# Performance work log

Measured on AMD Instinct MI355X. Metric: run time of the kernel, lower is better.

Reference implementation:

```python
import jax, jax.numpy as jnp
import numpy as np

B, S, L, H, VIN, VOUT = 64, 64, 64, 256, 10000, 10000


def setup_inputs() -> dict:
    key = jax.random.key(0)
    ks = jax.random.split(key, 14)
    f = lambda k, shp: jax.random.normal(k, shp, dtype=jnp.float32) * 0.05
    return {
        "X": f(ks[0], (B, S, VIN)),
        "ground_truth": jax.random.randint(ks[1], (B, L), 0, VOUT, dtype=jnp.int32),
        "enc_Wih": f(ks[2], (3 * H, VIN)),
        "enc_Whh": f(ks[3], (3 * H, H)),
        "enc_bih": f(ks[4], (3 * H,)),
        "enc_bhh": f(ks[5], (3 * H,)),
        "att_w": f(ks[6], (2 * H,)),
        "att_b": f(ks[7], ()),
        "dec_Wih": f(ks[8], (3 * H, H + VOUT)),
        "dec_Whh": f(ks[9], (3 * H, H)),
        "dec_bih": f(ks[10], (3 * H,)),
        "dec_bhh": f(ks[11], (3 * H,)),
        "out_W": f(ks[12], (VOUT, H)),
        "out_b": f(ks[13], (VOUT,)),
    }


def gru_cell(h, x, Wih, Whh, bih, bhh):
    # PyTorch GRU cell: gates ordered (r, z, n)
    gi = x @ Wih.T + bih          # [B, 3H]
    gh = h @ Whh.T + bhh          # [B, 3H]
    ir, iz, inn = jnp.split(gi, 3, axis=-1)
    hr, hz, hn = jnp.split(gh, 3, axis=-1)
    r = jax.nn.sigmoid(ir + hr)
    z = jax.nn.sigmoid(iz + hz)
    n = jnp.tanh(inn + r * hn)
    return (1.0 - z) * n + z * h


def reference(X, ground_truth, enc_Wih, enc_Whh, enc_bih, enc_bhh,
              att_w, att_b, dec_Wih, dec_Whh, dec_bih, dec_bhh, out_W, out_b):
    b = X.shape[0]
    h_dim = enc_Whh.shape[1]
    vout = out_W.shape[0]

    # ---- encoder GRU over time (time-major scan) ----
    Xs = jnp.transpose(X, (1, 0, 2))                      # [S, B, VIN]
    h0 = jnp.zeros((b, h_dim), X.dtype)

    def enc_step(h, x):
        h2 = gru_cell(h, x, enc_Wih, enc_Whh, enc_bih, enc_bhh)
        return h2, h2

    h_last, enc_h = jax.lax.scan(enc_step, h0, Xs)        # enc_h: [S, B, H]

    # additive attention: logits = relu(W_a [h_dec; enc_h] + b_a)
    w_dec, w_enc = jnp.split(att_w, 2)                    # each [H]
    enc_score = jnp.einsum('sbh,h->sb', enc_h, w_enc)     # precomputed, [S, B]

    gtT = ground_truth.T                                  # [L, B]
    prev0 = jnp.zeros((b, vout), X.dtype)                 # initial one-hot input (zeros)

    def dec_step(carry, gt_i):
        h, prev = carry
        logits = jax.nn.relu(enc_score + h @ w_dec + att_b)   # [S, B]
        wts = jax.nn.softmax(logits, axis=0)                  # softmax over enc positions
        ctx = jnp.einsum('sb,sbh->bh', wts, enc_h)            # [B, H]
        dec_in = jnp.concatenate([ctx, prev], axis=-1)        # [B, H + VOUT]
        h2 = gru_cell(h, dec_in, dec_Wih, dec_Whh, dec_bih, dec_bhh)
        logp = jax.nn.log_softmax(h2 @ out_W.T + out_b, axis=-1)  # [B, VOUT]
        onehot = jax.nn.one_hot(gt_i, vout, dtype=X.dtype)        # teacher forcing
        return (h2, onehot), logp

    _, outs = jax.lax.scan(dec_step, (h_last, prev0), gtT)    # [L, B, VOUT]
    return jnp.transpose(outs, (1, 0, 2))                     # [B, L, VOUT]
```

## Files before the change

kernel.cpp:

```cpp
#include <hip/hip_runtime.h>
#include <hip/hip_bf16.h>
#include <math.h>

#define NB 64
#define NS 64
#define NL 64
#define NH 256
#define G3 768
#define NVIN 10000
#define NVOUT 10000
#define KP2 10240
#define NOUTP 10112

typedef __attribute__((ext_vector_type(8))) short bf16x8;
typedef __attribute__((ext_vector_type(4))) float f32x4;
typedef __attribute__((ext_vector_type(4))) unsigned int u32x4;

__device__ __forceinline__ void gld_lds16(const __hip_bfloat16* g, __hip_bfloat16* l) {
  __builtin_amdgcn_global_load_lds(
      (const __attribute__((address_space(1))) unsigned int*)(const void*)g,
      (__attribute__((address_space(3))) unsigned int*)(void*)l, 16, 0, 0);
}

__device__ __forceinline__ unsigned int f2bf(float f) {
  unsigned int u = __float_as_uint(f);
  return (u + 0x7fff + ((u >> 16) & 1)) >> 16;
}

__device__ __forceinline__ float fast_tanh(float x) {
  float e = __expf(-2.f * x);
  return (1.f - e) / (1.f + e);
}

__global__ __launch_bounds__(256) void k_cvt_pad(
    const float* __restrict__ in, __hip_bfloat16* __restrict__ out,
    int in_rows, int in_cols, int out_cols, int swz) {
  int r = blockIdx.x;
  const float* src = in + (size_t)r * in_cols;
  __hip_bfloat16* dst = out + (size_t)r * out_cols;
  bool live = r < in_rows;
  int sx = swz ? ((r & 7) << 3) : 0;
  for (int c = threadIdx.x * 4; c < out_cols; c += 1024) {
    int cc = (c & ~63) | ((c & 63) ^ sx);
    __hip_bfloat16 v[4];
    if (live && cc + 3 < in_cols) {
      float4 f = *(const float4*)(src + cc);
      v[0] = __float2bfloat16(f.x); v[1] = __float2bfloat16(f.y);
      v[2] = __float2bfloat16(f.z); v[3] = __float2bfloat16(f.w);
    } else {
      v[0] = v[1] = v[2] = v[3] = __float2bfloat16(0.f);
    }
    *(ushort4*)(dst + c) = *(const ushort4*)v;
  }
}

__global__ __launch_bounds__(256) void k_wpack(
    const float* __restrict__ srcA, int strideA,
    const float* __restrict__ srcB, int strideB,
    __hip_bfloat16* __restrict__ out, int total) {
  int idx = blockIdx.x * 256 + threadIdx.x;
  if (idx >= total) return;
  int k = idx & 255, c = (idx >> 8) & 255, f = idx >> 16;
  float v = (f < 3) ? srcA[(size_t)(f * 256 + c) * strideA + k]
                    : srcB[(size_t)((f - 3) * 256 + c) * strideB + k];
  out[idx] = __float2bfloat16(v);
}

__global__ __launch_bounds__(256) void k_gemm_encS(
    const __hip_bfloat16* __restrict__ A, const __hip_bfloat16* __restrict__ B,
    float* __restrict__ P) {
  __shared__ __hip_bfloat16 As[128][64];
  __shared__ __hip_bfloat16 Bs[128][64];
  int t = threadIdx.x;
  int wid = t >> 6, lane = t & 63;
  int m0 = blockIdx.y * 128, n0 = blockIdx.x * 128;
  int wr = wid >> 1, wc = wid & 1;
  int r16 = lane & 15, hi16 = lane >> 4;
  int xr = (r16 & 7) << 4;
  f32x4 acc[4][4] = {};
  int kbeg = blockIdx.z * 2560;
  for (int ks = 0; ks < 40; ++ks) {
    int k0 = kbeg + ks * 64;
    __syncthreads();
#pragma unroll
    for (int is = 0; is < 4; ++is) {
      int off = is * 4096 + t * 16;
      int r = off >> 7, e = (off & 127) >> 1;
      gld_lds16(A + (size_t)(m0 + r) * KP2 + k0 + e, &As[r][e]);
      gld_lds16(B + (size_t)(n0 + r) * KP2 + k0 + e, &Bs[r][e]);
    }
    __syncthreads();
    const char* ab = (const char*)As;
    const char* bb = (const char*)Bs;
#pragma unroll
    for (int kk = 0; kk < 2; ++kk) {
      int ko = kk * 64 + hi16 * 16;
      bf16x8 af[4], bfr[4];
#pragma unroll
      for (int i = 0; i < 4; ++i) {
        af[i]  = *(const bf16x8*)(ab + (wr * 64 + i * 16 + r16) * 128 + (ko ^ xr));
        bfr[i] = *(const bf16x8*)(bb + (wc * 64 + i * 16 + r16) * 128 + (ko ^ xr));
      }
#pragma unroll
      for (int i = 0; i < 4; ++i)
#pragma unroll
        for (int j = 0; j < 4; ++j)
          acc[i][j] = __builtin_amdgcn_mfma_f32_16x16x32_bf16(af[i], bfr[j], acc[i][j], 0, 0, 0);
    }
  }
  float* Pz = P + (size_t)blockIdx.z * 4096 * G3;
#pragma unroll
  for (int i = 0; i < 4; ++i)
#pragma unroll
    for (int j = 0; j < 4; ++j) {
      int ccol = n0 + wc * 64 + j * 16 + r16;
#pragma unroll
      for (int q = 0; q < 4; ++q) {
        int crow = m0 + wr * 64 + i * 16 + hi16 * 4 + q;
        Pz[(size_t)crow * G3 + ccol] = acc[i][j][q];
      }
    }
}

__global__ __launch_bounds__(256) void k_reduce4(
    const float4* __restrict__ P, const float* __restrict__ bias,
    float4* __restrict__ G) {
  int idx = blockIdx.x * 256 + threadIdx.x;
  float4 a = P[idx], b = P[idx + 786432], c = P[idx + 2 * 786432],
         d = P[idx + 3 * 786432];
  float4 bs = *(const float4*)(bias + (idx % 192) * 4);
  float4 o;
  o.x = a.x + b.x + c.x + d.x + bs.x;
  o.y = a.y + b.y + c.y + d.y + bs.y;
  o.z = a.z + b.z + c.z + d.z + bs.z;
  o.w = a.w + b.w + c.w + d.w + bs.w;
  G[idx] = o;
}

__global__ __launch_bounds__(256) void k_gemm_outS(
    const __hip_bfloat16* __restrict__ A, const __hip_bfloat16* __restrict__ B,
    const float* __restrict__ bias, float* __restrict__ C) {
  __shared__ __hip_bfloat16 As[128][64];
  __shared__ __hip_bfloat16 Bs[128][64];
  int t = threadIdx.x;
  int wid = t >> 6, lane = t & 63;
  int m0 = blockIdx.y * 128, n0 = blockIdx.x * 128;
  int wr = wid >> 1, wc = wid & 1;
  int r16 = lane & 15, hi16 = lane >> 4;
  int xr = (r16 & 7) << 4;
  f32x4 acc[4][4] = {};
  for (int k0 = 0; k0 < NH; k0 += 64) {
    __syncthreads();
#pragma unroll
    for (int is = 0; is < 4; ++is) {
      int off = is * 4096 + t * 16;
      int r = off >> 7, e = (off & 127) >> 1;
      gld_lds16(A + (size_t)(m0 + r) * NH + k0 + e, &As[r][e]);
      gld_lds16(B + (size_t)(n0 + r) * NH + k0 + e, &Bs[r][e]);
    }
    __syncthreads();
    const char* ab = (const char*)As;
    const char* bb = (const char*)Bs;
#pragma unroll
    for (int kk = 0; kk < 2; ++kk) {
      int ko = kk * 64 + hi16 * 16;
      bf16x8 af[4], bfr[4];
#pragma unroll
      for (int i = 0; i < 4; ++i) {
        af[i]  = *(const bf16x8*)(ab + (wr * 64 + i * 16 + r16) * 128 + (ko ^ xr));
        bfr[i] = *(const bf16x8*)(bb + (wc * 64 + i * 16 + r16) * 128 + (ko ^ xr));
      }
#pragma unroll
      for (int i = 0; i < 4; ++i)
#pragma unroll
        for (int j = 0; j < 4; ++j)
          acc[i][j] = __builtin_amdgcn_mfma_f32_16x16x32_bf16(af[i], bfr[j], acc[i][j], 0, 0, 0);
    }
  }
#pragma unroll
  for (int i = 0; i < 4; ++i)
#pragma unroll
    for (int j = 0; j < 4; ++j) {
      int ccol = n0 + wc * 64 + j * 16 + r16;
      if (ccol < NVOUT) {
        float bs = bias[ccol];
#pragma unroll
        for (int q = 0; q < 4; ++q) {
          int crow = m0 + wr * 64 + i * 16 + hi16 * 4 + q;
          int l = crow >> 6, b = crow & 63;
          C[((size_t)b * NL + l) * NVOUT + ccol] = acc[i][j][q] + bs;
        }
      }
    }
}

__global__ __launch_bounds__(256) void k_gemm_encw(
    const __hip_bfloat16* __restrict__ A, const __hip_bfloat16* __restrict__ B,
    __hip_bfloat16* __restrict__ CT) {
  __shared__ __hip_bfloat16 As[128][32];
  __shared__ __hip_bfloat16 Bs[128][32];
  int t = threadIdx.x;
  int wid = t >> 6, lane = t & 63;
  int m0 = blockIdx.y * 128, n0 = blockIdx.x * 128;
  int wr = wid >> 1, wc = wid & 1;
  f32x4 acc[4][4] = {};
  for (int k0 = 0; k0 < NH; k0 += 32) {
    __syncthreads();
#pragma unroll
    for (int is = 0; is < 2; ++is) {
      int off = is * 4096 + wid * 1024 + lane * 16;
      int r = off >> 6, cb = (off & 63) >> 1;
      gld_lds16(A + (size_t)(m0 + r) * NH + k0 + cb, &As[r][cb]);
      gld_lds16(B + (size_t)(n0 + r) * NH + k0 + cb, &Bs[r][cb]);
    }
    __syncthreads();
    int r16 = lane & 15, kb = (lane >> 4) * 8;
    bf16x8 af[4], bfr[4];
#pragma unroll
    for (int i = 0; i < 4; ++i) {
      af[i]  = *(const bf16x8*)&As[wr * 64 + i * 16 + r16][kb];
      bfr[i] = *(const bf16x8*)&Bs[wc * 64 + i * 16 + r16][kb];
    }
#pragma unroll
    for (int i = 0; i < 4; ++i)
#pragma unroll
      for (int j = 0; j < 4; ++j)
        acc[i][j] = __builtin_amdgcn_mfma_f32_16x16x32_bf16(af[i], bfr[j], acc[i][j], 0, 0, 0);
  }
  int r16 = lane & 15, rg = lane >> 4;
#pragma unroll
  for (int i = 0; i < 4; ++i)
#pragma unroll
    for (int j = 0; j < 4; ++j) {
      int ccol = n0 + wc * 64 + j * 16 + r16;
#pragma unroll
      for (int q = 0; q < 4; ++q) {
        int crow = m0 + wr * 64 + i * 16 + rg * 4 + q;
        int bb = crow >> 6, ss = crow & 63;
        CT[((size_t)bb * G3 + ccol) * 64 + (ss ^ ((ccol & 7) << 3))] =
            __float2bfloat16(acc[i][j][q]);
      }
    }
}

__global__ __launch_bounds__(256) void k_pregather(
    const float* __restrict__ Wih, const float* __restrict__ bih,
    const int* __restrict__ gt, float* __restrict__ Gdec) {
  int ib = blockIdx.x;
  int i = ib >> 6, b = ib & 63;
  int tok = (i > 0) ? gt[b * NL + (i - 1)] : -1;
  for (int g = threadIdx.x; g < G3; g += 256) {
    float v = bih[g];
    if (tok >= 0) v += Wih[(size_t)g * (NH + NVOUT) + NH + tok];
    Gdec[(size_t)ib * G3 + g] = v;
  }
}

__global__ __launch_bounds__(512) void k_encoder4(
    const float* __restrict__ Gi, const __hip_bfloat16* __restrict__ Wcat,
    const float* __restrict__ bhh, const float* __restrict__ att_w,
    __hip_bfloat16* __restrict__ enchB, float* __restrict__ escoreT) {
  __shared__ float h32[2][256];
  __shared__ __hip_bfloat16 hbf[2][256];
  int t = threadIdx.x, w = t >> 6, lane = t & 63;
  int b = blockIdx.x;
  int r16 = lane & 15, hi16 = lane >> 4;
  bf16x8 wv[3][2][8];
#pragma unroll
  for (int f = 0; f < 3; ++f)
#pragma unroll
    for (int fc = 0; fc < 2; ++fc)
#pragma unroll
      for (int kf = 0; kf < 8; ++kf)
        wv[f][fc][kf] = *(const bf16x8*)(Wcat +
            (((size_t)f * 256 + w * 32 + fc * 16 + r16) * 256 + kf * 32 + hi16 * 8));
  float aw[4];
#pragma unroll
  for (int q = 0; q < 4; ++q) aw[q] = att_w[256 + lane + q * 64];
  if (t < 256) {
    h32[0][t] = 0.f; h32[1][t] = 0.f;
    hbf[0][t] = __float2bfloat16(0.f); hbf[1][t] = __float2bfloat16(0.f);
  }
  __syncthreads();
  int cur = 0;
  for (int s = 0; s < NS; ++s) {
    float gd[3][2];
    if (hi16 == 0) {
#pragma unroll
      for (int f = 0; f < 3; ++f)
#pragma unroll
        for (int fc = 0; fc < 2; ++fc)
          gd[f][fc] = Gi[((size_t)b * 64 + s) * G3 + f * 256 + w * 32 + fc * 16 + lane];
    }
    const char* hb = (const char*)&hbf[cur][0];
    f32x4 acc[3][2] = {};
#pragma unroll
    for (int half = 0; half < 2; ++half) {
      bf16x8 ah[4];
#pragma unroll
      for (int kf = 0; kf < 4; ++kf)
        ah[kf] = *(const bf16x8*)(hb + (half * 4 + kf) * 64 + hi16 * 16);
#pragma unroll
      for (int f = 0; f < 3; ++f)
#pragma unroll
        for (int fc = 0; fc < 2; ++fc)
#pragma unroll
          for (int kf = 0; kf < 4; ++kf)
            acc[f][fc] = __builtin_amdgcn_mfma_f32_16x16x32_bf16(
                ah[kf], wv[f][fc][half * 4 + kf], acc[f][fc], 0, 0, 0);
    }
    if (hi16 == 0) {
      int nxt = cur ^ 1;
#pragma unroll
      for (int fc = 0; fc < 2; ++fc) {
        int c = w * 32 + fc * 16 + lane;
        float rr = 1.f / (1.f + __expf(-(gd[0][fc] + acc[0][fc][0] + bhh[c])));
        float zz = 1.f / (1.f + __expf(-(gd[1][fc] + acc[1][fc][0] + bhh[256 + c])));
        float nn = fast_tanh(gd[2][fc] + rr * (acc[2][fc][0] + bhh[512 + c]));
        float hn = (1.f - zz) * nn + zz * h32[cur][c];
        h32[nxt][c] = hn;
        hbf[nxt][c] = __float2bfloat16(hn);
        enchB[((size_t)b * 64 + s) * 256 + c] = __float2bfloat16(hn);
      }
    }
    __syncthreads();
    cur ^= 1;
    if (w == 0) {
      float p = h32[cur][lane] * aw[0] + h32[cur][lane + 64] * aw[1]
              + h32[cur][lane + 128] * aw[2] + h32[cur][lane + 192] * aw[3];
#pragma unroll
      for (int off = 32; off; off >>= 1) p += __shfl_xor(p, off, 64);
      if (lane == 0) escoreT[(size_t)b * 64 + s] = p;
    }
  }
}

__global__ __launch_bounds__(512) void k_decoder6(
    const float* __restrict__ Gdec, const __hip_bfloat16* __restrict__ Wcat6,
    const float* __restrict__ bhh, const __hip_bfloat16* __restrict__ enchB,
    const __hip_bfloat16* __restrict__ ENCWT, const float* __restrict__ escoreT,
    const float* __restrict__ att_w, const float* __restrict__ att_b,
    __hip_bfloat16* __restrict__ dechb) {
  __shared__ __hip_bfloat16 encwT[G3][64];
  __shared__ __hip_bfloat16 hbf[2][256];
  __shared__ float h32[2][256];
  int t = threadIdx.x, w = t >> 6, lane = t & 63;
  int b = blockIdx.x;
  int r16 = lane & 15, hi16 = lane >> 4;
  int cw = w * 32;
  {
    const char* srcb = (const char*)(ENCWT + (size_t)b * G3 * 64);
    char* dstb = (char*)&encwT[0][0];
#pragma unroll
    for (int is = 0; is < 12; ++is) {
      int off = is * 8192 + t * 16;
      gld_lds16((const __hip_bfloat16*)(srcb + off), (__hip_bfloat16*)(dstb + off));
    }
  }
  bf16x8 wv[3][2][8];
#pragma unroll
  for (int f = 0; f < 3; ++f)
#pragma unroll
    for (int fc = 0; fc < 2; ++fc)
#pragma unroll
      for (int kf = 0; kf < 8; ++kf)
        wv[f][fc][kf] = *(const bf16x8*)(Wcat6 +
            (((size_t)(3 + f) * 256 + cw + fc * 16 + r16) * 256 + kf * 32 + hi16 * 8));
  float aw[4];
#pragma unroll
  for (int q = 0; q < 4; ++q) aw[q] = att_w[lane + q * 64];
  float attb = att_b[0];
  float esc = escoreT[(size_t)b * 64 + lane];
  float bh0[2], bh1[2], bh2[2];
#pragma unroll
  for (int fc = 0; fc < 2; ++fc) {
    bh0[fc] = bhh[cw + fc * 16 + r16];
    bh1[fc] = bhh[256 + cw + fc * 16 + r16];
    bh2[fc] = bhh[512 + cw + fc * 16 + r16];
  }
  u32x4 onesu = {0x3F803F80u, 0x3F803F80u, 0x3F803F80u, 0x3F803F80u};
  bf16x8 onesf = __builtin_bit_cast(bf16x8, onesu);
  if (t < 256) {
    float v = __bfloat162float(enchB[((size_t)b * 64 + 63) * 256 + t]);
    h32[0][t] = v;  hbf[0][t] = __float2bfloat16(v);
    h32[1][t] = 0.f; hbf[1][t] = __float2bfloat16(0.f);
  }
  __syncthreads();
  float hp[2];
  hp[0] = h32[0][cw + r16];
  hp[1] = h32[0][cw + 16 + r16];
  int bs3 = (b & 7) << 3;
  int cur = 0;
  for (int i = 0; i < NL; ++i) {
    float gd0[2], gd1[2], gd2[2];
    if (hi16 == 0) {
      const float* gp = Gdec + ((size_t)i * 64 + b) * G3;
#pragma unroll
      for (int fc = 0; fc < 2; ++fc) {
        gd0[fc] = gp[cw + fc * 16 + r16];
        gd1[fc] = gp[256 + cw + fc * 16 + r16];
        gd2[fc] = gp[512 + cw + fc * 16 + r16];
      }
    }
    const char* hb = (const char*)&hbf[cur][0];
    f32x4 acch[3][2] = {};
#pragma unroll
    for (int half = 0; half < 2; ++half) {
      bf16x8 ah[4];
#pragma unroll
      for (int kf = 0; kf < 4; ++kf)
        ah[kf] = *(const bf16x8*)(hb + (half * 4 + kf) * 64 + hi16 * 16);
#pragma unroll
      for (int f = 0; f < 3; ++f)
#pragma unroll
        for (int fc = 0; fc < 2; ++fc)
#pragma unroll
          for (int kf = 0; kf < 4; ++kf)
            acch[f][fc] = __builtin_amdgcn_mfma_f32_16x16x32_bf16(
                ah[kf], wv[f][fc][half * 4 + kf], acch[f][fc], 0, 0, 0);
    }
    float p = h32[cur][lane] * aw[0] + h32[cur][lane + 64] * aw[1]
            + h32[cur][lane + 128] * aw[2] + h32[cur][lane + 192] * aw[3];
#pragma unroll
    for (int off = 32; off; off >>= 1) p += __shfl_xor(p, off, 64);
    float lg = fmaxf(esc + p + attb, 0.f);
    float e = __expf(lg);
    bf16x8 af_[2];
#pragma unroll
    for (int kf = 0; kf < 2; ++kf) {
      u32x4 tmp;
#pragma unroll
      for (int j = 0; j < 4; ++j) {
        int src = hi16 * 8 + kf * 32 + 2 * j;
        tmp[j] = f2bf(__shfl(e, src, 64)) | (f2bf(__shfl(e, src + 1, 64)) << 16);
      }
      af_[kf] = __builtin_bit_cast(bf16x8, tmp);
    }
    f32x4 smacc = {};
    smacc = __builtin_amdgcn_mfma_f32_16x16x32_bf16(af_[0], onesf, smacc, 0, 0, 0);
    smacc = __builtin_amdgcn_mfma_f32_16x16x32_bf16(af_[1], onesf, smacc, 0, 0, 0);
    f32x4 acci[3][2] = {};
    const char* eb = (const char*)&encwT[0][0];
#pragma unroll
    for (int g = 0; g < 3; ++g)
#pragma unroll
      for (int fc = 0; fc < 2; ++fc) {
        int cloc = g * 256 + cw + fc * 16 + r16;
        int xb = (cloc & 7) << 4;
#pragma unroll
        for (int kf = 0; kf < 2; ++kf) {
          bf16x8 bfrag = *(const bf16x8*)(eb + cloc * 128 + ((kf * 64 + hi16 * 16) ^ xb));
          acci[g][fc] = __builtin_amdgcn_mfma_f32_16x16x32_bf16(
              af_[kf], bfrag, acci[g][fc], 0, 0, 0);
        }
      }
    if (hi16 == 0) {
      float rn = 1.f / smacc[0];
      int nxt = cur ^ 1;
#pragma unroll
      for (int fc = 0; fc < 2; ++fc) {
        int c = cw + fc * 16 + r16;
        float rr = 1.f / (1.f + __expf(-(gd0[fc] + acci[0][fc][0] * rn + acch[0][fc][0] + bh0[fc])));
        float zz = 1.f / (1.f + __expf(-(gd1[fc] + acci[1][fc][0] * rn + acch[1][fc][0] + bh1[fc])));
        float nn = fast_tanh(gd2[fc] + acci[2][fc][0] * rn + rr * (acch[2][fc][0] + bh2[fc]));
        float hn = (1.f - zz) * nn + zz * hp[fc];
        hp[fc] = hn;
        h32[nxt][c] = hn;
        hbf[nxt][c] = __float2bfloat16(hn);
        int cs = (c & ~63) | ((c & 63) ^ bs3);
        dechb[((size_t)i * 64 + b) * 256 + cs] = __float2bfloat16(hn);
      }
    }
    __syncthreads();
    cur ^= 1;
  }
}

__global__ __launch_bounds__(256) void k_logsoftmax(float* __restrict__ out) {
  float* x = out + (size_t)blockIdx.x * NVOUT;
  __shared__ float red[256];
  int t = threadIdx.x;
  float4 v[10];
  float mx = -1e30f;
#pragma unroll
  for (int ii = 0; ii < 10; ++ii) {
    int slot = ii * 256 + t;
    if (slot < 2500) {
      v[ii] = *(const float4*)(x + slot * 4);
      mx = fmaxf(mx, fmaxf(fmaxf(v[ii].x, v[ii].y), fmaxf(v[ii].z, v[ii].w)));
    }
  }
  red[t] = mx; __syncthreads();
  for (int off = 128; off; off >>= 1) {
    if (t < off) red[t] = fmaxf(red[t], red[t + off]);
    __syncthreads();
  }
  mx = red[0]; __syncthreads();
  float sm = 0.f;
#pragma unroll
  for (int ii = 0; ii < 10; ++ii) {
    int slot = ii * 256 + t;
    if (slot < 2500)
      sm += __expf(v[ii].x - mx) + __expf(v[ii].y - mx)
          + __expf(v[ii].z - mx) + __expf(v[ii].w - mx);
  }
  red[t] = sm; __syncthreads();
  for (int off = 128; off; off >>= 1) {
    if (t < off) red[t] += red[t + off];
    __syncthreads();
  }
  float lse = mx + logf(red[0]);
#pragma unroll
  for (int ii = 0; ii < 10; ++ii) {
    int slot = ii * 256 + t;
    if (slot < 2500) {
      float4 o; o.x = v[ii].x - lse; o.y = v[ii].y - lse;
      o.z = v[ii].z - lse; o.w = v[ii].w - lse;
      *(float4*)(x + slot * 4) = o;
    }
  }
}

extern "C" void kernel_launch(void* const* d_in, const int* in_sizes, int n_in,
                              void* d_out, int out_size, void* d_ws, size_t ws_size,
                              hipStream_t stream) {
  const float* X        = (const float*)d_in[0];
  const int*   gt       = (const int*)  d_in[1];
  const float* enc_Wih  = (const float*)d_in[2];
  const float* enc_Whh  = (const float*)d_in[3];
  const float* enc_bih  = (const float*)d_in[4];
  const float* enc_bhh  = (const float*)d_in[5];
  const float* att_w    = (const float*)d_in[6];
  const float* att_b    = (const float*)d_in[7];
  const float* dec_Wih  = (const float*)d_in[8];
  const float* dec_Whh  = (const float*)d_in[9];
  const float* dec_bih  = (const float*)d_in[10];
  const float* dec_bhh  = (const float*)d_in[11];
  const float* out_W    = (const float*)d_in[12];
  const float* out_b    = (const float*)d_in[13];
  float* out = (float*)d_out;

  float* p = (float*)d_ws;
  float* Gienc  = p; p += NS * NB * G3;
  float* Gdec   = p; p += NL * NB * G3;
  float* escoreT = p; p += NB * NS;
  __hip_bfloat16* q = (__hip_bfloat16*)p;
  __hip_bfloat16* enchBb = q; q += (size_t)NB * NS * NH;
  __hip_bfloat16* Wcat_e = q; q += (size_t)3 * 256 * 256;
  __hip_bfloat16* Wcat_d = q; q += (size_t)6 * 256 * 256;
  __hip_bfloat16* Xb     = q; q += (size_t)4096 * KP2;
  __hip_bfloat16* Wencb  = q; q += (size_t)G3 * KP2;
  __hip_bfloat16* Woutb  = q; q += (size_t)NOUTP * NH;
  __hip_bfloat16* dechb  = q; q += (size_t)NL * NB * NH;
  __hip_bfloat16* ENCWT  = (__hip_bfloat16*)Gienc;
  float* Pout = (float*)d_out;

  k_cvt_pad<<<4096, 256, 0, stream>>>(X, Xb, 4096, NVIN, KP2, 1);
  k_cvt_pad<<<G3, 256, 0, stream>>>(enc_Wih, Wencb, G3, NVIN, KP2, 1);
  k_cvt_pad<<<NOUTP, 256, 0, stream>>>(out_W, Woutb, NVOUT, NH, NH, 1);
  k_wpack<<<768, 256, 0, stream>>>(enc_Whh, NH, enc_Whh, NH, Wcat_e, 3 * 65536);
  k_wpack<<<1536, 256, 0, stream>>>(dec_Wih, NH + NVOUT, dec_Whh, NH, Wcat_d, 6 * 65536);
  k_pregather<<<NL * NB, 256, 0, stream>>>(dec_Wih, dec_bih, gt, Gdec);

  k_gemm_encS<<<dim3(6, 32, 4), 256, 0, stream>>>(Xb, Wencb, Pout);
  k_reduce4<<<3072, 256, 0, stream>>>((const float4*)Pout, enc_bih, (float4*)Gienc);
  k_encoder4<<<64, 512, 0, stream>>>(Gienc, Wcat_e, enc_bhh, att_w, enchBb, escoreT);
  k_gemm_encw<<<dim3(6, 32), 256, 0, stream>>>(enchBb, Wcat_d, ENCWT);
  k_decoder6<<<64, 512, 0, stream>>>(Gdec, Wcat_d, dec_bhh, enchBb, ENCWT,
                                     escoreT, att_w, att_b, dechb);
  k_gemm_outS<<<dim3(79, 32), 256, 0, stream>>>(dechb, Woutb, out_b, out);
  k_logsoftmax<<<NB * NL, 256, 0, stream>>>(out);
}
```

Measured before the change: 789.4 us.

## Trim serial recurrence critical path in encoder and decoder GRU loops

```diff
diff --git a/kernel.cpp b/kernel.cpp
--- a/kernel.cpp
+++ b/kernel.cpp
@@ -30,6 +30,10 @@
 __device__ __forceinline__ float fast_tanh(float x) {
   float e = __expf(-2.f * x);
   return (1.f - e) / (1.f + e);
+}
+
+__device__ __forceinline__ void lds_barrier() {
+  asm volatile("s_waitcnt lgkmcnt(0)\n\ts_barrier" ::: "memory");
 }
 
 __global__ __launch_bounds__(256) void k_cvt_pad(
@@ -256,15 +260,14 @@
   }
 }
 
-__global__ __launch_bounds__(512) void k_encoder4(
+__global__ __launch_bounds__(512) void k_encoder5(
     const float* __restrict__ Gi, const __hip_bfloat16* __restrict__ Wcat,
-    const float* __restrict__ bhh, const float* __restrict__ att_w,
-    __hip_bfloat16* __restrict__ enchB, float* __restrict__ escoreT) {
-  __shared__ float h32[2][256];
+    const float* __restrict__ bhh, __hip_bfloat16* __restrict__ enchB) {
   __shared__ __hip_bfloat16 hbf[2][256];
   int t = threadIdx.x, w = t >> 6, lane = t & 63;
   int b = blockIdx.x;
   int r16 = lane & 15, hi16 = lane >> 4;
+  int cw = w * 32;
   bf16x8 wv[3][2][8];
 #pragma unroll
   for (int f = 0; f < 3; ++f)
@@ -273,24 +276,31 @@
 #pragma unroll
       for (int kf = 0; kf < 8; ++kf)
         wv[f][fc][kf] = *(const bf16x8*)(Wcat +
-            (((size_t)f * 256 + w * 32 + fc * 16 + r16) * 256 + kf * 32 + hi16 * 8));
-  float aw[4];
-#pragma unroll
-  for (int q = 0; q < 4; ++q) aw[q] = att_w[256 + lane + q * 64];
+            (((size_t)f * 256 + cw + fc * 16 + r16) * 256 + kf * 32 + hi16 * 8));
+  float bh0[2], bh1[2], bh2[2];
+#pragma unroll
+  for (int fc = 0; fc < 2; ++fc) {
+    bh0[fc] = bhh[cw + fc * 16 + r16];
+    bh1[fc] = bhh[256 + cw + fc * 16 + r16];
+    bh2[fc] = bhh[512 + cw + fc * 16 + r16];
+  }
   if (t < 256) {
-    h32[0][t] = 0.f; h32[1][t] = 0.f;
-    hbf[0][t] = __float2bfloat16(0.f); hbf[1][t] = __float2bfloat16(0.f);
+    hbf[0][t] = __float2bfloat16(0.f);
+    hbf[1][t] = __float2bfloat16(0.f);
   }
   __syncthreads();
+  float hp[2] = {0.f, 0.f};
   int cur = 0;
   for (int s = 0; s < NS; ++s) {
-    float gd[3][2];
+    float gd0[2], gd1[2], gd2[2];
     if (hi16 == 0) {
-#pragma unroll
-      for (int f = 0; f < 3; ++f)
-#pragma unroll
-        for (int fc = 0; fc < 2; ++fc)
-          gd[f][fc] = Gi[((size_t)b * 64 + s) * G3 + f * 256 + w * 32 + fc * 16 + lane];
+      const float* gp = Gi + ((size_t)b * 64 + s) * G3;
+#pragma unroll
+      for (int fc = 0; fc < 2; ++fc) {
+        gd0[fc] = gp[cw + fc * 16 + r16];
+        gd1[fc] = gp[256 + cw + fc * 16 + r16];
+        gd2[fc] = gp[512 + cw + fc * 16 + r16];
+      }
     }
     const char* hb = (const char*)&hbf[cur][0];
     f32x4 acc[3][2] = {};
@@ -313,37 +323,46 @@
       int nxt = cur ^ 1;
 #pragma unroll
       for (int fc = 0; fc < 2; ++fc) {
-        int c = w * 32 + fc * 16 + lane;
-        float rr = 1.f / (1.f + __expf(-(gd[0][fc] + acc[0][fc][0] + bhh[c])));
-        float zz = 1.f / (1.f + __expf(-(gd[1][fc] + acc[1][fc][0] + bhh[256 + c])));
-        float nn = fast_tanh(gd[2][fc] + rr * (acc[2][fc][0] + bhh[512 + c]));
-        float hn = (1.f - zz) * nn + zz * h32[cur][c];
-        h32[nxt][c] = hn;
+        int c = cw + fc * 16 + r16;
+        float rr = 1.f / (1.f + __expf(-(gd0[fc] + acc[0][fc][0] + bh0[fc])));
+        float zz = 1.f / (1.f + __expf(-(gd1[fc] + acc[1][fc][0] + bh1[fc])));
+        float nn = fast_tanh(gd2[fc] + rr * (acc[2][fc][0] + bh2[fc]));
+        float hn = (1.f - zz) * nn + zz * hp[fc];
+        hp[fc] = hn;
         hbf[nxt][c] = __float2bfloat16(hn);
         enchB[((size_t)b * 64 + s) * 256 + c] = __float2bfloat16(hn);
       }
     }
-    __syncthreads();
+    lds_barrier();
     cur ^= 1;
-    if (w == 0) {
-      float p = h32[cur][lane] * aw[0] + h32[cur][lane + 64] * aw[1]
-              + h32[cur][lane + 128] * aw[2] + h32[cur][lane + 192] * aw[3];
-#pragma unroll
-      for (int off = 32; off; off >>= 1) p += __shfl_xor(p, off, 64);
-      if (lane == 0) escoreT[(size_t)b * 64 + s] = p;
-    }
-  }
-}
-
-__global__ __launch_bounds__(512) void k_decoder6(
+  }
+}
+
+__global__ __launch_bounds__(256) void k_escoreB(
+    const __hip_bfloat16* __restrict__ enchB, const float* __restrict__ att_w,
+    float* __restrict__ escoreT) {
+  int row = blockIdx.x * 4 + (threadIdx.x >> 6);
+  int lane = threadIdx.x & 63;
+  ushort4 u = *(const ushort4*)(enchB + (size_t)row * 256 + lane * 4);
+  const float* we = att_w + 256 + lane * 4;
+  float p = __uint_as_float((unsigned)u.x << 16) * we[0]
+          + __uint_as_float((unsigned)u.y << 16) * we[1]
+          + __uint_as_float((unsigned)u.z << 16) * we[2]
+          + __uint_as_float((unsigned)u.w << 16) * we[3];
+#pragma unroll
+  for (int off = 32; off; off >>= 1) p += __shfl_xor(p, off, 64);
+  if (lane == 0) escoreT[row] = p;
+}
+
+__global__ __launch_bounds__(512) void k_decoder7(
     const float* __restrict__ Gdec, const __hip_bfloat16* __restrict__ Wcat6,
     const float* __restrict__ bhh, const __hip_bfloat16* __restrict__ enchB,
     const __hip_bfloat16* __restrict__ ENCWT, const float* __restrict__ escoreT,
     const float* __restrict__ att_w, const float* __restrict__ att_b,
     __hip_bfloat16* __restrict__ dechb) {
-  __shared__ __hip_bfloat16 encwT[G3][64];
+  __shared__ __hip_bfloat16 encwT[G3 + 8][64];
   __shared__ __hip_bfloat16 hbf[2][256];
-  __shared__ float h32[2][256];
+  __shared__ float psumL[2][8];
   int t = threadIdx.x, w = t >> 6, lane = t & 63;
   int b = blockIdx.x;
   int r16 = lane & 15, hi16 = lane >> 4;
@@ -357,6 +376,10 @@
       gld_lds16((const __hip_bfloat16*)(srcb + off), (__hip_bfloat16*)(dstb + off));
     }
   }
+  {
+    unsigned* op = (unsigned*)&encwT[768][0];
+    if (t < 32) op[t] = 0x3F803F80u;
+  }
   bf16x8 wv[3][2][8];
 #pragma unroll
   for (int f = 0; f < 3; ++f)
@@ -366,9 +389,7 @@
       for (int kf = 0; kf < 8; ++kf)
         wv[f][fc][kf] = *(const bf16x8*)(Wcat6 +
             (((size_t)(3 + f) * 256 + cw + fc * 16 + r16) * 256 + kf * 32 + hi16 * 8));
-  float aw[4];
-#pragma unroll
-  for (int q = 0; q < 4; ++q) aw[q] = att_w[lane + q * 64];
+  float wd0 = att_w[cw + r16], wd1 = att_w[cw + 16 + r16];
   float attb = att_b[0];
   float esc = escoreT[(size_t)b * 64 + lane];
   float bh0[2], bh1[2], bh2[2];
@@ -378,17 +399,20 @@
     bh1[fc] = bhh[256 + cw + fc * 16 + r16];
     bh2[fc] = bhh[512 + cw + fc * 16 + r16];
   }
-  u32x4 onesu = {0x3F803F80u, 0x3F803F80u, 0x3F803F80u, 0x3F803F80u};
-  bf16x8 onesf = __builtin_bit_cast(bf16x8, onesu);
   if (t < 256) {
-    float v = __bfloat162float(enchB[((size_t)b * 64 + 63) * 256 + t]);
-    h32[0][t] = v;  hbf[0][t] = __float2bfloat16(v);
-    h32[1][t] = 0.f; hbf[1][t] = __float2bfloat16(0.f);
+    hbf[0][t] = enchB[((size_t)b * 64 + 63) * 256 + t];
+    hbf[1][t] = __float2bfloat16(0.f);
+  }
+  float hp[2];
+  hp[0] = __bfloat162float(enchB[((size_t)b * 64 + 63) * 256 + cw + r16]);
+  hp[1] = __bfloat162float(enchB[((size_t)b * 64 + 63) * 256 + cw + 16 + r16]);
+  if (hi16 == 0) {
+    float pp = hp[0] * wd0 + hp[1] * wd1;
+    pp += __shfl_xor(pp, 1, 64); pp += __shfl_xor(pp, 2, 64);
+    pp += __shfl_xor(pp, 4, 64); pp += __shfl_xor(pp, 8, 64);
+    if (lane == 0) psumL[0][w] = pp;
   }
   __syncthreads();
-  float hp[2];
-  hp[0] = h32[0][cw + r16];
-  hp[1] = h32[0][cw + 16 + r16];
   int bs3 = (b & 7) << 3;
   int cur = 0;
   for (int i = 0; i < NL; ++i) {
@@ -403,26 +427,22 @@
       }
     }
     const char* hb = (const char*)&hbf[cur][0];
+    bf16x8 ah[8];
+#pragma unroll
+    for (int kf = 0; kf < 8; ++kf)
+      ah[kf] = *(const bf16x8*)(hb + kf * 64 + hi16 * 16);
+    float4 pa = *(const float4*)&psumL[cur][0];
+    float4 pb = *(const float4*)&psumL[cur][4];
+    float p = ((pa.x + pa.y) + (pa.z + pa.w)) + ((pb.x + pb.y) + (pb.z + pb.w));
     f32x4 acch[3][2] = {};
 #pragma unroll
-    for (int half = 0; half < 2; ++half) {
-      bf16x8 ah[4];
-#pragma unroll
-      for (int kf = 0; kf < 4; ++kf)
-        ah[kf] = *(const bf16x8*)(hb + (half * 4 + kf) * 64 + hi16 * 16);
-#pragma unroll
-      for (int f = 0; f < 3; ++f)
-#pragma unroll
-        for (int fc = 0; fc < 2; ++fc)
-#pragma unroll
-          for (int kf = 0; kf < 4; ++kf)
-            acch[f][fc] = __builtin_amdgcn_mfma_f32_16x16x32_bf16(
-                ah[kf], wv[f][fc][half * 4 + kf], acch[f][fc], 0, 0, 0);
-    }
-    float p = h32[cur][lane] * aw[0] + h32[cur][lane + 64] * aw[1]
-            + h32[cur][lane + 128] * aw[2] + h32[cur][lane + 192] * aw[3];
-#pragma unroll
-    for (int off = 32; off; off >>= 1) p += __shfl_xor(p, off, 64);
+    for (int f = 0; f < 3; ++f)
+#pragma unroll
+      for (int fc = 0; fc < 2; ++fc)
+#pragma unroll
+        for (int kf = 0; kf < 8; ++kf)
+          acch[f][fc] = __builtin_amdgcn_mfma_f32_16x16x32_bf16(
+              ah[kf], wv[f][fc][kf], acch[f][fc], 0, 0, 0);
     float lg = fmaxf(esc + p + attb, 0.f);
     float e = __expf(lg);
     bf16x8 af_[2];
@@ -436,10 +456,8 @@
       }
       af_[kf] = __builtin_bit_cast(bf16x8, tmp);
     }
-    f32x4 smacc = {};
-    smacc = __builtin_amdgcn_mfma_f32_16x16x32_bf16(af_[0], onesf, smacc, 0, 0, 0);
-    smacc = __builtin_amdgcn_mfma_f32_16x16x32_bf16(af_[1], onesf, smacc, 0, 0, 0);
     f32x4 acci[3][2] = {};
+    f32x4 accs = {};
     const char* eb = (const char*)&encwT[0][0];
 #pragma unroll
     for (int g = 0; g < 3; ++g)
@@ -454,9 +472,15 @@
               af_[kf], bfrag, acci[g][fc], 0, 0, 0);
         }
       }
+#pragma unroll
+    for (int kf = 0; kf < 2; ++kf) {
+      bf16x8 ofrag = *(const bf16x8*)(eb + 768 * 128 + kf * 64 + hi16 * 16);
+      accs = __builtin_amdgcn_mfma_f32_16x16x32_bf16(af_[kf], ofrag, accs, 0, 0, 0);
+    }
     if (hi16 == 0) {
-      float rn = 1.f / smacc[0];
+      float rn = 1.f / accs[0];
       int nxt = cur ^ 1;
+      float hn2[2];
 #pragma unroll
       for (int fc = 0; fc < 2; ++fc) {
         int c = cw + fc * 16 + r16;
@@ -464,14 +488,17 @@
         float zz = 1.f / (1.f + __expf(-(gd1[fc] + acci[1][fc][0] * rn + acch[1][fc][0] + bh1[fc])));
         float nn = fast_tanh(gd2[fc] + acci[2][fc][0] * rn + rr * (acch[2][fc][0] + bh2[fc]));
         float hn = (1.f - zz) * nn + zz * hp[fc];
-        hp[fc] = hn;
-        h32[nxt][c] = hn;
+        hp[fc] = hn; hn2[fc] = hn;
         hbf[nxt][c] = __float2bfloat16(hn);
         int cs = (c & ~63) | ((c & 63) ^ bs3);
         dechb[((size_t)i * 64 + b) * 256 + cs] = __float2bfloat16(hn);
       }
-    }
-    __syncthreads();
+      float pp = hn2[0] * wd0 + hn2[1] * wd1;
+      pp += __shfl_xor(pp, 1, 64); pp += __shfl_xor(pp, 2, 64);
+      pp += __shfl_xor(pp, 4, 64); pp += __shfl_xor(pp, 8, 64);
+      if (lane == 0) psumL[cur ^ 1][w] = pp;
+    }
+    lds_barrier();
     cur ^= 1;
   }
 }
@@ -564,9 +591,10 @@
 
   k_gemm_encS<<<dim3(6, 32, 4), 256, 0, stream>>>(Xb, Wencb, Pout);
   k_reduce4<<<3072, 256, 0, stream>>>((const float4*)Pout, enc_bih, (float4*)Gienc);
-  k_encoder4<<<64, 512, 0, stream>>>(Gienc, Wcat_e, enc_bhh, att_w, enchBb, escoreT);
+  k_encoder5<<<64, 512, 0, stream>>>(Gienc, Wcat_e, enc_bhh, enchBb);
+  k_escoreB<<<1024, 256, 0, stream>>>(enchBb, att_w, escoreT);
   k_gemm_encw<<<dim3(6, 32), 256, 0, stream>>>(enchBb, Wcat_d, ENCWT);
-  k_decoder6<<<64, 512, 0, stream>>>(Gdec, Wcat_d, dec_bhh, enchBb, ENCWT,
+  k_decoder7<<<64, 512, 0, stream>>>(Gdec, Wcat_d, dec_bhh, enchBb, ENCWT,
                                      escoreT, att_w, att_b, dechb);
   k_gemm_outS<<<dim3(79, 32), 256, 0, stream>>>(dechb, Woutb, out_b, out);
   k_logsoftmax<<<NB * NL, 256, 0, stream>>>(out);
```

Measured after the change: 733.8 us. 1.08x faster.
